# Performance work log

Hardware: AMD Instinct MI355X
Metric: run time of the kernel (lower is better)

## Reference

```python
import jax, jax.numpy as jnp
import numpy as np

N_E = 8192
E_DIM = 256
BETA = 0.25


def setup_inputs() -> dict:
    key = jax.random.key(0)
    k1, k2 = jax.random.split(key)
    z = jax.random.normal(k1, (16, 1024, E_DIM), dtype=jnp.float32)
    # matches embedding.weight.data.uniform_(-1/n_e, 1/n_e)
    embedding = jax.random.uniform(k2, (N_E, E_DIM), dtype=jnp.float32,
                                   minval=-1.0 / N_E, maxval=1.0 / N_E)
    return {"z": z, "embedding": embedding}


def reference(z, embedding):
    B, S, D = z.shape  # [16, 1024, 256]
    zf = z.reshape(-1, D)  # [N, D], N = B*S
    # squared L2 distances to every codebook entry: [N, n_e]
    d = (jnp.sum(zf * zf, axis=1, keepdims=True)
         + jnp.sum(embedding * embedding, axis=1)
         - 2.0 * (zf @ embedding.T))
    min_encoding_indices = jnp.argmin(d, axis=1)  # [N]
    # one-hot encodings (returned by the module) [N, n_e]
    min_encodings = jax.nn.one_hot(min_encoding_indices, N_E, dtype=jnp.float32)
    # z_q = min_encodings @ embedding == gather of nearest codes
    z_q = embedding[min_encoding_indices].reshape(z.shape)  # [B, S, D]
    sg = jax.lax.stop_gradient
    loss = jnp.mean((sg(z_q) - z) ** 2) + BETA * jnp.mean((z_q - sg(z)) ** 2)
    # straight-through estimator
    z_q_st = z + sg(z_q - z)
    e_mean = jnp.mean(min_encodings, axis=0)  # [n_e]
    perplexity = jnp.exp(-jnp.sum(e_mean * jnp.log(e_mean + 1e-10)))
    return (loss, z_q_st, perplexity, min_encodings, min_encoding_indices[:, None])
```

## Files before the change

kernel.cpp:

```cpp
#include <hip/hip_runtime.h>
#include <cstddef>

#define NROWS 16384
#define NE    8192
#define DD    256

typedef unsigned long long u64;
typedef float vf4 __attribute__((ext_vector_type(4)));
typedef short bf16x8 __attribute__((ext_vector_type(8)));
typedef float f32x4 __attribute__((ext_vector_type(4)));
typedef unsigned short us8 __attribute__((ext_vector_type(8)));

#define OH_TOT ((size_t)NROWS * NE)
#define OH_VEC ((OH_TOT - 4) / 4)
#define CAND_CAP 4000000
#define LLIST_CAP 2048

__global__ __launch_bounds__(256) void k_rowsq(
    const float* __restrict__ z, const float* __restrict__ emb,
    float* __restrict__ zsq, float* __restrict__ esq,
    u64* __restrict__ best, int* __restrict__ counts,
    float* __restrict__ wadd, int* __restrict__ cand_n,
    unsigned short* __restrict__ ebf)
{
  const int g = blockIdx.x * 256 + threadIdx.x;
  if (g == 0) *cand_n = 0;
  if (g < NE) counts[g] = 0;
  if (g < NROWS) best[g] = ~0ull;

  const float* row;
  float* outp;
  if (g < NROWS) { row = z + (size_t)g * DD;            outp = zsq + g; }
  else           { row = emb + (size_t)(g - NROWS) * DD; outp = esq + (g - NROWS); }

  float sa = 0.0f;
  float half_s[2];
#pragma unroll
  for (int h = 0; h < 2; ++h) {
    const float* p = row + h * 128;
    float r[8];
    {
      const float4 v0 = *(const float4*)(p);
      const float4 v1 = *(const float4*)(p + 4);
      const float xs[8] = {v0.x, v0.y, v0.z, v0.w, v1.x, v1.y, v1.z, v1.w};
#pragma unroll
      for (int j = 0; j < 8; ++j) {
        float sq = xs[j] * xs[j];
        asm volatile("" : "+v"(sq));
        r[j] = sq;
        sa += fabsf(xs[j]);
      }
    }
    for (int i = 8; i < 128; i += 8) {
      const float4 v0 = *(const float4*)(p + i);
      const float4 v1 = *(const float4*)(p + i + 4);
      const float xs[8] = {v0.x, v0.y, v0.z, v0.w, v1.x, v1.y, v1.z, v1.w};
#pragma unroll
      for (int j = 0; j < 8; ++j) {
        float sq = xs[j] * xs[j];
        asm volatile("" : "+v"(sq));
        r[j] = r[j] + sq;
        sa += fabsf(xs[j]);
      }
    }
    half_s[h] = ((r[0] + r[1]) + (r[2] + r[3])) + ((r[4] + r[5]) + (r[6] + r[7]));
  }
  const float zs = half_s[0] + half_s[1];
  *outp = zs;
  if (g < NROWS) {
    wadd[g] = 2.0f * ((zs + 2.0f) * 1.2e-7f + 2.0f * (1.0e-6f * sa) + 5.0e-8f);
  } else {
    const int c = g - NROWS;
    const int t = c >> 4, l = c & 15;
#pragma unroll
    for (int kt = 0; kt < 8; ++kt) {
#pragma unroll
      for (int kq = 0; kq < 4; ++kq) {
        const float4 v0 = *(const float4*)(row + kt * 32 + kq * 8);
        const float4 v1 = *(const float4*)(row + kt * 32 + kq * 8 + 4);
        const float xs[8] = {v0.x, v0.y, v0.z, v0.w, v1.x, v1.y, v1.z, v1.w};
        us8 u;
#pragma unroll
        for (int j = 0; j < 8; ++j) {
          const unsigned b = __float_as_uint(xs[j]);
          u[j] = (unsigned short)((b + 0x7FFFu + ((b >> 16) & 1u)) >> 16);
        }
        *(us8*)(ebf + (((size_t)(t * 8 + kt)) * 64 + kq * 16 + l) * 8) = u;
      }
    }
  }
}

__device__ __forceinline__ unsigned short f2bf_rne(float f) {
  const unsigned u = __float_as_uint(f);
  return (unsigned short)((u + 0x7FFFu + ((u >> 16) & 1u)) >> 16);
}
__device__ __forceinline__ unsigned encf(float f) {
  const unsigned u = __float_as_uint(f);
  return (u & 0x80000000u) ? ~u : (u | 0x80000000u);
}
__device__ __forceinline__ float decf(unsigned k) {
  const unsigned u = (k & 0x80000000u) ? (k ^ 0x80000000u) : ~k;
  return __uint_as_float(u);
}

__global__ __launch_bounds__(256) void k_screen(
    const float* __restrict__ z, const unsigned short* __restrict__ ebf,
    const float* __restrict__ esq, const float* __restrict__ wadd,
    unsigned* __restrict__ cand, int* __restrict__ cand_n,
    float* __restrict__ ohbase)
{
  __shared__ unsigned smin[128];
  __shared__ float wl[128];
  __shared__ unsigned llist[LLIST_CAP];
  __shared__ unsigned lcnt;
  __shared__ unsigned gbase;

  const int tid = threadIdx.x;
  const int b = blockIdx.x;
  const int eighth = b & 7;
  const int panel = b >> 3;
  const int R0 = panel * 128;
  const int C0 = eighth * 1024;
  const int T0 = C0 >> 4;

  const int wave = tid >> 6;
  const int lane = tid & 63;
  const int l15 = lane & 15;
  const int kg = lane >> 4;

  if (tid < 128) { smin[tid] = 0xFFFFFFFFu; wl[tid] = wadd[R0 + tid]; }
  if (tid == 0) lcnt = 0;

  bf16x8 af0[8], af1[8];
  {
    const float* zp0 = z + (size_t)(R0 + wave * 32 + l15) * DD + kg * 8;
    const float* zp1 = zp0 + 16 * DD;
#pragma unroll
    for (int kt = 0; kt < 8; ++kt) {
      const float4 a0 = *(const float4*)(zp0 + kt * 32);
      const float4 a1 = *(const float4*)(zp0 + kt * 32 + 4);
      const float4 c0 = *(const float4*)(zp1 + kt * 32);
      const float4 c1 = *(const float4*)(zp1 + kt * 32 + 4);
      bf16x8 w, v;
      w[0] = (short)f2bf_rne(a0.x); w[1] = (short)f2bf_rne(a0.y);
      w[2] = (short)f2bf_rne(a0.z); w[3] = (short)f2bf_rne(a0.w);
      w[4] = (short)f2bf_rne(a1.x); w[5] = (short)f2bf_rne(a1.y);
      w[6] = (short)f2bf_rne(a1.z); w[7] = (short)f2bf_rne(a1.w);
      v[0] = (short)f2bf_rne(c0.x); v[1] = (short)f2bf_rne(c0.y);
      v[2] = (short)f2bf_rne(c0.z); v[3] = (short)f2bf_rne(c0.w);
      v[4] = (short)f2bf_rne(c1.x); v[5] = (short)f2bf_rne(c1.y);
      v[6] = (short)f2bf_rne(c1.z); v[7] = (short)f2bf_rne(c1.w);
      af0[kt] = w;
      af1[kt] = v;
    }
  }
  __syncthreads();

  const int rbase = wave * 32 + kg * 4;
  const bf16x8* fb = (const bf16x8*)ebf;

  float rm[8];
#pragma unroll
  for (int i = 0; i < 8; ++i) rm[i] = 1e30f;
#pragma unroll 1
  for (int tt = 0; tt < 64; ++tt) {
    bf16x8 bfr[8];
#pragma unroll
    for (int kt = 0; kt < 8; ++kt)
      bfr[kt] = fb[(size_t)((T0 + tt) * 8 + kt) * 64 + lane];
    f32x4 e0 = (f32x4){0, 0, 0, 0}, o0 = (f32x4){0, 0, 0, 0};
    f32x4 e1 = (f32x4){0, 0, 0, 0}, o1 = (f32x4){0, 0, 0, 0};
#pragma unroll
    for (int kt = 0; kt < 8; kt += 2) {
      e0 = __builtin_amdgcn_mfma_f32_16x16x32_bf16(af0[kt], bfr[kt], e0, 0, 0, 0);
      o0 = __builtin_amdgcn_mfma_f32_16x16x32_bf16(af0[kt + 1], bfr[kt + 1], o0, 0, 0, 0);
      e1 = __builtin_amdgcn_mfma_f32_16x16x32_bf16(af1[kt], bfr[kt], e1, 0, 0, 0);
      o1 = __builtin_amdgcn_mfma_f32_16x16x32_bf16(af1[kt + 1], bfr[kt + 1], o1, 0, 0, 0);
    }
    const float ev = esq[C0 + tt * 16 + l15];
#pragma unroll
    for (int r = 0; r < 4; ++r) {
      rm[r]     = fminf(rm[r],     ev - 2.0f * (e0[r] + o0[r]));
      rm[4 + r] = fminf(rm[4 + r], ev - 2.0f * (e1[r] + o1[r]));
    }
  }
#pragma unroll
  for (int rs = 0; rs < 2; ++rs)
#pragma unroll
    for (int r = 0; r < 4; ++r) {
      float mn = rm[rs * 4 + r];
      mn = fminf(mn, __shfl_xor(mn, 1, 16));
      mn = fminf(mn, __shfl_xor(mn, 2, 16));
      mn = fminf(mn, __shfl_xor(mn, 4, 16));
      mn = fminf(mn, __shfl_xor(mn, 8, 16));
      if (l15 == 0) atomicMin(&smin[rbase + rs * 16 + r], encf(mn));
    }
  __syncthreads();

  float thr[8];
#pragma unroll
  for (int rs = 0; rs < 2; ++rs)
#pragma unroll
    for (int r = 0; r < 4; ++r) {
      const int R = rbase + rs * 16 + r;
      thr[rs * 4 + r] = decf(smin[R]) + wl[R];
    }

#define PUSH(E_)                                                            \
  {                                                                         \
    const unsigned s_ = atomicAdd(&lcnt, 1u);                               \
    if (s_ < LLIST_CAP) llist[s_] = (E_);                                   \
    else { const int g_ = atomicAdd(cand_n, 1);                             \
           if (g_ < CAND_CAP) cand[g_] = (E_); }                            \
  }

#pragma unroll 1
  for (int tt = 0; tt < 64; ++tt) {
    bf16x8 bfr[8];
#pragma unroll
    for (int kt = 0; kt < 8; ++kt)
      bfr[kt] = fb[(size_t)((T0 + tt) * 8 + kt) * 64 + lane];
    f32x4 e0 = (f32x4){0, 0, 0, 0}, o0 = (f32x4){0, 0, 0, 0};
    f32x4 e1 = (f32x4){0, 0, 0, 0}, o1 = (f32x4){0, 0, 0, 0};
#pragma unroll
    for (int kt = 0; kt < 8; kt += 2) {
      e0 = __builtin_amdgcn_mfma_f32_16x16x32_bf16(af0[kt], bfr[kt], e0, 0, 0, 0);
      o0 = __builtin_amdgcn_mfma_f32_16x16x32_bf16(af0[kt + 1], bfr[kt + 1], o0, 0, 0, 0);
      e1 = __builtin_amdgcn_mfma_f32_16x16x32_bf16(af1[kt], bfr[kt], e1, 0, 0, 0);
      o1 = __builtin_amdgcn_mfma_f32_16x16x32_bf16(af1[kt + 1], bfr[kt + 1], o1, 0, 0, 0);
    }
    const int c = C0 + tt * 16 + l15;
    const float ev = esq[c];
    float rv[8];
    float gm = 1e30f;
#pragma unroll
    for (int r = 0; r < 4; ++r) {
      rv[r]     = ev - 2.0f * (e0[r] + o0[r]);
      rv[4 + r] = ev - 2.0f * (e1[r] + o1[r]);
      gm = fminf(gm, rv[r] - thr[r]);
      gm = fminf(gm, rv[4 + r] - thr[4 + r]);
    }
    if (gm <= 0.0f) {
#pragma unroll
      for (int rs = 0; rs < 2; ++rs)
#pragma unroll
        for (int r = 0; r < 4; ++r)
          if (rv[rs * 4 + r] <= thr[rs * 4 + r])
            PUSH(((unsigned)(R0 + rbase + rs * 16 + r) << 13) | (unsigned)c);
    }
  }

  __syncthreads();
  const unsigned n = (lcnt < LLIST_CAP) ? lcnt : LLIST_CAP;
  if (tid == 0) gbase = (unsigned)atomicAdd(cand_n, (int)n);
  __syncthreads();
  for (unsigned i = tid; i < n; i += 256) {
    const unsigned g = gbase + i;
    if (g < CAND_CAP) cand[g] = llist[i];
  }

  {
    const vf4 zz = {0.0f, 0.0f, 0.0f, 0.0f};
    float* zp = ohbase + 2;
    size_t zt = (size_t)b * 32768 + tid;
#pragma unroll 4
    for (int i = 0; i < 128; ++i) {
      if (zt < OH_VEC) __builtin_nontemporal_store(zz, (vf4*)(zp + 4 * zt));
      zt += 256;
    }
    if (b == 0 && tid == 0) { ohbase[0] = 0.0f; ohbase[1] = 0.0f; }
    if (b == 1023 && tid == 0) { ohbase[OH_TOT - 2] = 0.0f; ohbase[OH_TOT - 1] = 0.0f; }
  }
}

__global__ __launch_bounds__(256) void k_recheck(
    const float* __restrict__ z, const float* __restrict__ emb,
    const float* __restrict__ zsq, const float* __restrict__ esq,
    const unsigned* __restrict__ cand, const int* __restrict__ cand_n,
    u64* __restrict__ best)
{
  const int n = min(*cand_n, CAND_CAP);
  for (int i = blockIdx.x * 256 + threadIdx.x; i < n; i += gridDim.x * 256) {
    const unsigned e = cand[i];
    const int row = (int)(e >> 13);
    const int col = (int)(e & (NE - 1));
    const float4* zr = (const float4*)(z + (size_t)row * DD);
    const float4* er = (const float4*)(emb + (size_t)col * DD);
    float dot = 0.0f;
#pragma unroll 8
    for (int q = 0; q < 64; ++q) {
      const float4 a = zr[q];
      const float4 b = er[q];
      dot = fmaf(a.x, b.x, dot);
      dot = fmaf(a.y, b.y, dot);
      dot = fmaf(a.z, b.z, dot);
      dot = fmaf(a.w, b.w, dot);
    }
    const float s1 = zsq[row] + esq[col];
    const float dv = s1 - 2.0f * dot;
    atomicMin(&best[row], ((u64)__float_as_uint(dv) << 32) | (unsigned)col);
  }
}

__global__ __launch_bounds__(256) void k_gather2(
    const float* __restrict__ z, const float* __restrict__ emb,
    const u64* __restrict__ best,
    float* __restrict__ out_zq, float* __restrict__ out_onehot,
    float* __restrict__ out_idx, float* __restrict__ partials,
    int* __restrict__ counts)
{
  __shared__ float sred[256];
  const int row = blockIdx.x * 4 + (threadIdx.x >> 6);
  const int lane = threadIdx.x & 63;
  const int idx = (int)(unsigned)(best[row] & 0xffffffffull);
  const int k0 = lane * 4;

  const float4 e  = *(const float4*)(emb + (size_t)idx * DD + k0);
  const float4 zv = *(const float4*)(z + (size_t)row * DD + k0);
  *(float4*)(out_zq + (size_t)row * DD + k0) = e;

  const float dx = e.x - zv.x, dy = e.y - zv.y, dz = e.z - zv.z, dw = e.w - zv.w;
  sred[threadIdx.x] = dx * dx + dy * dy + dz * dz + dw * dw;

  if (lane == 0) {
    out_idx[row] = (float)idx;
    out_onehot[(size_t)row * NE + idx] = 1.0f;
    atomicAdd(&counts[idx], 1);
  }
  __syncthreads();
  for (int s = 128; s > 0; s >>= 1) {
    if (threadIdx.x < s) sred[threadIdx.x] += sred[threadIdx.x + s];
    __syncthreads();
  }
  if (threadIdx.x == 0) partials[blockIdx.x] = sred[0];
}

__global__ __launch_bounds__(256) void k_final(
    const int* __restrict__ counts, const float* __restrict__ partials,
    float* __restrict__ out_loss, float* __restrict__ out_perp)
{
  __shared__ float sred[256];
  __shared__ float sl[256];
  float le = 0.0f;
  for (int e = threadIdx.x; e < NE; e += 256) {
    const float p = (float)counts[e] * (1.0f / 16384.0f);
    le += p * logf(p + 1e-10f);
  }
  float ll = 0.0f;
  for (int b = threadIdx.x; b < NROWS / 4; b += 256) ll += partials[b];
  sred[threadIdx.x] = le;
  sl[threadIdx.x] = ll;
  __syncthreads();
  for (int s = 128; s > 0; s >>= 1) {
    if (threadIdx.x < s) {
      sred[threadIdx.x] += sred[threadIdx.x + s];
      sl[threadIdx.x] += sl[threadIdx.x + s];
    }
    __syncthreads();
  }
  if (threadIdx.x == 0) {
    *out_perp = expf(-sred[0]);
    *out_loss = sl[0] * (1.25f / 4194304.0f);
  }
}

extern "C" void kernel_launch(void* const* d_in, const int* in_sizes, int n_in,
                              void* d_out, int out_size, void* d_ws, size_t ws_size,
                              hipStream_t stream) {
  const float* z   = (const float*)d_in[0];
  const float* emb = (const float*)d_in[1];

  float* out        = (float*)d_out;
  float* out_loss   = out;
  float* out_zq     = out + 1;
  float* out_perp   = out + 4194305;
  float* out_onehot = out + 4194306;
  float* out_idx    = out + 138412034;

  float* zsq      = (float*)d_ws;
  float* esq      = zsq + NROWS;
  u64*   best     = (u64*)(esq + NE);
  int*   counts   = (int*)(best + NROWS);
  float* partials = (float*)(counts + NE);
  float* wadd     = partials + 4096;
  int*   cand_n   = (int*)(wadd + NROWS);
  unsigned short* ebf = (unsigned short*)(wadd + NROWS + 4);
  unsigned* cand  = (unsigned*)(ebf + (size_t)NE * DD);

  k_rowsq<<<96, 256, 0, stream>>>(z, emb, zsq, esq, best, counts, wadd, cand_n, ebf);
  k_screen<<<1024, 256, 0, stream>>>(z, ebf, esq, wadd, cand, cand_n, out_onehot);
  k_recheck<<<512, 256, 0, stream>>>(z, emb, zsq, esq, cand, cand_n, best);
  k_gather2<<<NROWS / 4, 256, 0, stream>>>(z, emb, best, out_zq, out_onehot,
                                           out_idx, partials, counts);
  k_final<<<1, 256, 0, stream>>>(counts, partials, out_loss, out_perp);
}
```

Before: 975.8 us.

## Stage codebook tiles through LDS with double-buffered async global loads

The screen kernel used to have every wave load the same bf16 codebook fragments from global memory on its own. Each block now loads a 16-code tile once into a double-buffered LDS area using global_load_lds. The load for the next tile is issued while the MFMAs for the current tile run. This removes redundant global and L2 traffic across the four waves, at the cost of 16KB of LDS and a block barrier every iteration. The barrier after the z-fragment setup is merged into the initial staging barrier, and the prefetch is not explicitly waited on before the barrier, which depends on the compiler inserting vmcnt waits.

```diff
diff --git a/kernel.cpp b/kernel.cpp
--- a/kernel.cpp
+++ b/kernel.cpp
@@ -104,12 +104,19 @@
   return __uint_as_float(u);
 }
 
+__device__ __forceinline__ void gload_lds16(const void* g, void* l) {
+  __builtin_amdgcn_global_load_lds(
+      (const __attribute__((address_space(1))) unsigned int*)g,
+      (__attribute__((address_space(3))) unsigned int*)l, 16, 0, 0);
+}
+
 __global__ __launch_bounds__(256) void k_screen(
     const float* __restrict__ z, const unsigned short* __restrict__ ebf,
     const float* __restrict__ esq, const float* __restrict__ wadd,
     unsigned* __restrict__ cand, int* __restrict__ cand_n,
     float* __restrict__ ohbase)
 {
+  __shared__ __align__(16) unsigned char Bs[2][8192];
   __shared__ unsigned smin[128];
   __shared__ float wl[128];
   __shared__ unsigned llist[LLIST_CAP];
@@ -155,35 +162,53 @@
       af1[kt] = v;
     }
   }
-  __syncthreads();
 
   const int rbase = wave * 32 + kg * 4;
-  const bf16x8* fb = (const bf16x8*)ebf;
+  const unsigned char* fbyte = (const unsigned char*)ebf;
+
+#define SSTAGE(B_, TT_)                                                     \
+  {                                                                         \
+    const unsigned char* gs = fbyte +                                       \
+        (((size_t)((T0 + (TT_)) * 8 + wave * 2) * 64 + lane) << 4);         \
+    gload_lds16(gs, &Bs[B_][(wave * 2) * 1024]);                            \
+    gload_lds16(gs + 1024, &Bs[B_][(wave * 2 + 1) * 1024]);                 \
+  }
+
+#define LOADB(B_, BFR_)                                                     \
+  _Pragma("unroll")                                                         \
+  for (int fi = 0; fi < 8; ++fi)                                            \
+    BFR_[fi] = *(const bf16x8*)&Bs[B_][fi * 1024 + lane * 16];
+
+#define MFMA16(BFR_, E0_, O0_, E1_, O1_)                                    \
+  _Pragma("unroll")                                                         \
+  for (int kt = 0; kt < 8; kt += 2) {                                       \
+    E0_ = __builtin_amdgcn_mfma_f32_16x16x32_bf16(af0[kt], BFR_[kt], E0_, 0, 0, 0);         \
+    O0_ = __builtin_amdgcn_mfma_f32_16x16x32_bf16(af0[kt + 1], BFR_[kt + 1], O0_, 0, 0, 0); \
+    E1_ = __builtin_amdgcn_mfma_f32_16x16x32_bf16(af1[kt], BFR_[kt], E1_, 0, 0, 0);         \
+    O1_ = __builtin_amdgcn_mfma_f32_16x16x32_bf16(af1[kt + 1], BFR_[kt + 1], O1_, 0, 0, 0); \
+  }
 
   float rm[8];
 #pragma unroll
   for (int i = 0; i < 8; ++i) rm[i] = 1e30f;
+
+  SSTAGE(0, 0);
+  __syncthreads();
 #pragma unroll 1
   for (int tt = 0; tt < 64; ++tt) {
+    if (tt + 1 < 64) SSTAGE((tt + 1) & 1, tt + 1);
     bf16x8 bfr[8];
-#pragma unroll
-    for (int kt = 0; kt < 8; ++kt)
-      bfr[kt] = fb[(size_t)((T0 + tt) * 8 + kt) * 64 + lane];
+    LOADB(tt & 1, bfr);
     f32x4 e0 = (f32x4){0, 0, 0, 0}, o0 = (f32x4){0, 0, 0, 0};
     f32x4 e1 = (f32x4){0, 0, 0, 0}, o1 = (f32x4){0, 0, 0, 0};
-#pragma unroll
-    for (int kt = 0; kt < 8; kt += 2) {
-      e0 = __builtin_amdgcn_mfma_f32_16x16x32_bf16(af0[kt], bfr[kt], e0, 0, 0, 0);
-      o0 = __builtin_amdgcn_mfma_f32_16x16x32_bf16(af0[kt + 1], bfr[kt + 1], o0, 0, 0, 0);
-      e1 = __builtin_amdgcn_mfma_f32_16x16x32_bf16(af1[kt], bfr[kt], e1, 0, 0, 0);
-      o1 = __builtin_amdgcn_mfma_f32_16x16x32_bf16(af1[kt + 1], bfr[kt + 1], o1, 0, 0, 0);
-    }
+    MFMA16(bfr, e0, o0, e1, o1);
     const float ev = esq[C0 + tt * 16 + l15];
 #pragma unroll
     for (int r = 0; r < 4; ++r) {
       rm[r]     = fminf(rm[r],     ev - 2.0f * (e0[r] + o0[r]));
       rm[4 + r] = fminf(rm[4 + r], ev - 2.0f * (e1[r] + o1[r]));
     }
+    __syncthreads();
   }
 #pragma unroll
   for (int rs = 0; rs < 2; ++rs)
@@ -215,21 +240,16 @@
            if (g_ < CAND_CAP) cand[g_] = (E_); }                            \
   }
 
+  SSTAGE(0, 0);
+  __syncthreads();
 #pragma unroll 1
   for (int tt = 0; tt < 64; ++tt) {
+    if (tt + 1 < 64) SSTAGE((tt + 1) & 1, tt + 1);
     bf16x8 bfr[8];
-#pragma unroll
-    for (int kt = 0; kt < 8; ++kt)
-      bfr[kt] = fb[(size_t)((T0 + tt) * 8 + kt) * 64 + lane];
+    LOADB(tt & 1, bfr);
     f32x4 e0 = (f32x4){0, 0, 0, 0}, o0 = (f32x4){0, 0, 0, 0};
     f32x4 e1 = (f32x4){0, 0, 0, 0}, o1 = (f32x4){0, 0, 0, 0};
-#pragma unroll
-    for (int kt = 0; kt < 8; kt += 2) {
-      e0 = __builtin_amdgcn_mfma_f32_16x16x32_bf16(af0[kt], bfr[kt], e0, 0, 0, 0);
-      o0 = __builtin_amdgcn_mfma_f32_16x16x32_bf16(af0[kt + 1], bfr[kt + 1], o0, 0, 0, 0);
-      e1 = __builtin_amdgcn_mfma_f32_16x16x32_bf16(af1[kt], bfr[kt], e1, 0, 0, 0);
-      o1 = __builtin_amdgcn_mfma_f32_16x16x32_bf16(af1[kt + 1], bfr[kt + 1], o1, 0, 0, 0);
-    }
+    MFMA16(bfr, e0, o0, e1, o1);
     const int c = C0 + tt * 16 + l15;
     const float ev = esq[c];
     float rv[8];
@@ -249,9 +269,9 @@
           if (rv[rs * 4 + r] <= thr[rs * 4 + r])
             PUSH(((unsigned)(R0 + rbase + rs * 16 + r) << 13) | (unsigned)c);
     }
-  }
-
-  __syncthreads();
+    __syncthreads();
+  }
+
   const unsigned n = (lcnt < LLIST_CAP) ? lcnt : LLIST_CAP;
   if (tid == 0) gbase = (unsigned)atomicAdd(cand_n, (int)n);
   __syncthreads();
```

Result: faster. 952.3 us (-2.4%).
